# Performance work log

Measured on AMD Instinct MI355X. Metric: run time of the kernel, lower is better.

## Reference

```python
import jax, jax.numpy as jnp
import numpy as np
import math

B, S, D = 1, 2048, 2048
NQ, NKV = 32, 8
HD = D // NQ            # 64
NREP = NQ // NKV        # 4
EPS = 1e-6


def _rope_tables(seq_len, head_dim, theta=10000.0):
    half = head_dim // 2
    inv_freq = 1.0 / (theta ** (np.arange(0, half, dtype=np.float32) / half))
    t = np.arange(seq_len, dtype=np.float32)
    freqs = np.outer(t, inv_freq)  # [S, half]
    return jnp.asarray(np.cos(freqs)), jnp.asarray(np.sin(freqs))


def _rmsnorm(x, g, eps=EPS):
    denom = jnp.sqrt(jnp.mean(x * x, axis=-1, keepdims=True) + eps)
    return x / denom * g


def _rope(x, cos, sin):
    # x: [B, S, H, HD]; cos/sin: [S, HD//2]
    half = x.shape[-1] // 2
    x1, x2 = x[..., :half], x[..., half:]
    c = cos[None, :, None, :]
    s = sin[None, :, None, :]
    return jnp.concatenate([x1 * c - x2 * s, x1 * s + x2 * c], axis=-1)


def setup_inputs() -> dict:
    key = jax.random.key(0)
    ks = jax.random.split(key, 6)
    scale = 1.0 / math.sqrt(D)
    x = jax.random.normal(ks[0], (B, S, D), dtype=jnp.float32)
    Wq = jax.random.normal(ks[1], (D, NQ * HD), dtype=jnp.float32) * scale
    Wk = jax.random.normal(ks[2], (D, NKV * HD), dtype=jnp.float32) * scale
    Wv = jax.random.normal(ks[3], (D, NKV * HD), dtype=jnp.float32) * scale
    Wo = jax.random.normal(ks[4], (NQ * HD, D), dtype=jnp.float32) * scale
    g_q = jnp.ones((HD,), dtype=jnp.float32)
    g_k = jnp.ones((HD,), dtype=jnp.float32)
    cos, sin = _rope_tables(S, HD)
    return {"x": x, "cos": cos, "sin": sin, "g_q": g_q, "g_k": g_k,
            "Wq": Wq, "Wk": Wk, "Wv": Wv, "Wo": Wo}


def reference(x, cos, sin, g_q, g_k, Wq, Wk, Wv, Wo):
    bs, seq, _ = x.shape
    Q = (x @ Wq).reshape(bs, seq, NQ, HD)
    K = (x @ Wk).reshape(bs, seq, NKV, HD)
    V = (x @ Wv).reshape(bs, seq, NKV, HD)
    Q = _rope(_rmsnorm(Q, g_q), cos, sin)
    K = _rope(_rmsnorm(K, g_k), cos, sin)
    # GQA: repeat_interleave KV heads to match Q heads
    K = jnp.repeat(K, NREP, axis=2)  # [B,S,NQ,HD]
    V = jnp.repeat(V, NREP, axis=2)
    # scores: [B, H, S, S]
    scores = jnp.einsum('bshd,bthd->bhst', Q, K) / math.sqrt(HD)
    mask = jnp.triu(jnp.ones((seq, seq), dtype=bool), k=1)
    scores = jnp.where(mask, -jnp.inf, scores)
    attn = jax.nn.softmax(scores, axis=-1)
    out = jnp.einsum('bhst,bthd->bshd', attn, V).reshape(bs, seq, NQ * HD)
    return out @ Wo
```

## Files before the change

### kernel.cpp

```cpp
#include <hip/hip_runtime.h>
#include <hip/hip_bf16.h>
#include <math.h>

#define S 2048
#define D 2048
#define NQ 32
#define NKV 8
#define HD 64
#define HALF 32
#define NREP 4
#define QKV_N 3072
#define KCOL 2048
#define VCOL 2560

typedef unsigned short ushort_t;
typedef __attribute__((ext_vector_type(8))) short bf16x8;
typedef __attribute__((ext_vector_type(4))) float f32x4;
typedef float f4 __attribute__((ext_vector_type(4)));

__device__ __forceinline__ ushort_t f2bf(float f) {
    __hip_bfloat16 h = __float2bfloat16(f);
    return *reinterpret_cast<ushort_t*>(&h);
}
__device__ __forceinline__ float bf2f(ushort_t u) {
    __hip_bfloat16 h = *reinterpret_cast<__hip_bfloat16*>(&u);
    return __bfloat162float(h);
}

__device__ __forceinline__ void load_lds16(const ushort_t* g, ushort_t* l) {
    __builtin_amdgcn_global_load_lds(
        (const __attribute__((address_space(1))) unsigned int*)g,
        (__attribute__((address_space(3))) unsigned int*)l,
        16, 0, 0);
}

__global__ __launch_bounds__(256) void prep_all(const float* __restrict__ x,
                                                ushort_t* __restrict__ Xb,
                                                const float* __restrict__ Wq,
                                                const float* __restrict__ Wk,
                                                const float* __restrict__ Wv,
                                                ushort_t* __restrict__ WqkvT) {
    __shared__ float tile[32][33];
    const int b = blockIdx.x;
    if (b < 4096) {
        int i = (b * 256 + threadIdx.x) * 4;
        f4 v = *(const f4*)&x[i];
        Xb[i + 0] = f2bf(v[0]);
        Xb[i + 1] = f2bf(v[1]);
        Xb[i + 2] = f2bf(v[2]);
        Xb[i + 3] = f2bf(v[3]);
        return;
    }
    const float* src; int N, row_off, t;
    if (b < 8192)      { src = Wq; N = 2048; row_off = 0;    t = b - 4096; }
    else if (b < 9216) { src = Wk; N = 512;  row_off = 2048; t = b - 8192; }
    else               { src = Wv; N = 512;  row_off = 2560; t = b - 9216; }
    const int ntn = N / 32;
    const int n0 = (t % ntn) * 32, k0 = (t / ntn) * 32;
    const int tx = threadIdx.x & 31, ty = threadIdx.x >> 5;
    #pragma unroll
    for (int i = 0; i < 32; i += 8)
        tile[ty + i][tx] = src[(size_t)(k0 + ty + i) * N + (n0 + tx)];
    __syncthreads();
    #pragma unroll
    for (int i = 0; i < 32; i += 8)
        WqkvT[(size_t)(row_off + n0 + ty + i) * 2048 + (k0 + tx)] = f2bf(tile[tx][ty + i]);
}

template <typename OutT>
__global__ __launch_bounds__(256) void gemm64(const ushort_t* __restrict__ A,
                                              const ushort_t* __restrict__ BT,
                                              OutT* __restrict__ C,
                                              int M, int N, int Kdim) {
    __shared__ ushort_t As[64][64];
    __shared__ ushort_t Bs[64][64];
    const int tid = threadIdx.x;
    const int w = tid >> 6, lane = tid & 63;
    const int r16 = lane & 15, quad = lane >> 4;
    const int wm = (w >> 1) * 32, wn = (w & 1) * 32;
    const int bm = blockIdx.y * 64, bn = blockIdx.x * 64;
    const int srow = lane >> 3;
    const int jl = (lane & 7) ^ srow;
    const int rx = r16 & 7;

    f32x4 acc[2][2];
    #pragma unroll
    for (int r = 0; r < 2; ++r)
        #pragma unroll
        for (int c = 0; c < 2; ++c) acc[r][c] = (f32x4){0.f, 0.f, 0.f, 0.f};

    for (int k0 = 0; k0 < Kdim; k0 += 64) {
        __syncthreads();
        #pragma unroll
        for (int i = 0; i < 2; ++i) {
            int rbase = w * 16 + i * 8;
            load_lds16(A  + (size_t)(bm + rbase + srow) * Kdim + k0 + jl * 8, &As[rbase][0]);
            load_lds16(BT + (size_t)(bn + rbase + srow) * Kdim + k0 + jl * 8, &Bs[rbase][0]);
        }
        __syncthreads();

        #pragma unroll
        for (int h = 0; h < 2; ++h) {
            bf16x8 af[2], bfr[2];
            #pragma unroll
            for (int r = 0; r < 2; ++r)
                af[r]  = *(const bf16x8*)&As[wm + 16 * r + r16][((quad + 4 * h) ^ rx) * 8];
            #pragma unroll
            for (int c = 0; c < 2; ++c)
                bfr[c] = *(const bf16x8*)&Bs[wn + 16 * c + r16][((quad + 4 * h) ^ rx) * 8];
            #pragma unroll
            for (int r = 0; r < 2; ++r)
                #pragma unroll
                for (int c = 0; c < 2; ++c)
                    acc[r][c] = __builtin_amdgcn_mfma_f32_16x16x32_bf16(af[r], bfr[c], acc[r][c], 0, 0, 0);
        }
    }

    #pragma unroll
    for (int r = 0; r < 2; ++r)
        #pragma unroll
        for (int c = 0; c < 2; ++c)
            #pragma unroll
            for (int reg = 0; reg < 4; ++reg) {
                int row = bm + wm + 16 * r + quad * 4 + reg;
                int col = bn + wn + 16 * c + r16;
                float v = acc[r][c][reg];
                if constexpr (sizeof(OutT) == 2) C[(size_t)row * N + col] = (OutT)f2bf(v);
                else                             C[(size_t)row * N + col] = (OutT)v;
            }
}

__global__ __launch_bounds__(256) void rms_rope_vwo(ushort_t* __restrict__ QKV,
                                                    const float* __restrict__ gq,
                                                    const float* __restrict__ gk,
                                                    const float* __restrict__ cosT,
                                                    const float* __restrict__ sinT,
                                                    ushort_t* __restrict__ VTg,
                                                    const float* __restrict__ Wo,
                                                    ushort_t* __restrict__ WoT) {
    const int y = blockIdx.y, xb = blockIdx.x;
    if (y < 10) {
        const int s = xb;
        const int w = threadIdx.x >> 6;
        const int hh = y * 4 + w;
        const int d = threadIdx.x & 63;
        const float* g;
        int col;
        if (hh < NQ) { g = gq; col = hh * HD; }
        else         { g = gk; col = KCOL + (hh - NQ) * HD; }
        ushort_t* xp = QKV + (size_t)s * QKV_N + col;
        float v = bf2f(xp[d]);
        float ss = v * v;
        #pragma unroll
        for (int off = 32; off > 0; off >>= 1) ss += __shfl_down(ss, off);
        ss = __shfl(ss, 0);
        float inv = rsqrtf(ss * (1.0f / HD) + 1e-6f);
        float xn = v * inv * g[d];
        float other = __shfl(xn, d ^ 32);
        float c = cosT[(size_t)s * HALF + (d & 31)];
        float sn = sinT[(size_t)s * HALF + (d & 31)];
        float outv = (d < HALF) ? (xn * c - other * sn) : (other * sn + xn * c);
        xp[d] = f2bf(outv);
        return;
    }
    const int tx = threadIdx.x & 31, ty = threadIdx.x >> 5;
    if (y == 10 && xb < 1024) {
        __shared__ ushort_t vt[32][33];
        const int s0 = (xb & 63) * 32, d0 = (xb >> 6) * 32;
        #pragma unroll
        for (int i = 0; i < 32; i += 8)
            vt[ty + i][tx] = QKV[(size_t)(s0 + ty + i) * QKV_N + VCOL + d0 + tx];
        __syncthreads();
        #pragma unroll
        for (int i = 0; i < 32; i += 8)
            VTg[(size_t)(d0 + ty + i) * S + s0 + tx] = vt[tx][ty + i];
        return;
    }
    int idx;
    if (y == 10)      idx = xb - 1024;
    else if (y == 11) idx = 1024 + xb;
    else              idx = 3072 + xb;
    if (idx < 0 || idx >= 4096) return;
    __shared__ float wt[32][33];
    const int n0 = (idx & 63) * 32, k0 = (idx >> 6) * 32;
    #pragma unroll
    for (int i = 0; i < 32; i += 8)
        wt[ty + i][tx] = Wo[(size_t)(k0 + ty + i) * 2048 + (n0 + tx)];
    __syncthreads();
    #pragma unroll
    for (int i = 0; i < 32; i += 8)
        WoT[(size_t)(n0 + ty + i) * 2048 + (k0 + tx)] = f2bf(wt[tx][ty + i]);
}

__global__ __launch_bounds__(256) void zero_acc(f4* __restrict__ AccBuf4,
                                                f4* __restrict__ AccL4) {
    int i = blockIdx.x * 256 + threadIdx.x;
    if (i < 524288) AccBuf4[i] = (f4){0.f, 0.f, 0.f, 0.f};
    else if (i < 532480) AccL4[i - 524288] = (f4){0.f, 0.f, 0.f, 0.f};
}

__global__ __launch_bounds__(256) void flash_attn_mfma(const ushort_t* __restrict__ QKV,
                                                       const ushort_t* __restrict__ VTg,
                                                       ushort_t* __restrict__ O,
                                                       float* __restrict__ AccBuf,
                                                       float* __restrict__ AccL) {
    __shared__ ushort_t Ks[2][32][64];
    __shared__ ushort_t Vt[2][64][32];
    __shared__ ushort_t Ps[4][16][40];

    const int bx = blockIdx.x;
    int qt, tb, te;
    bool atom;
    if (bx < 16) { qt = 16 + bx; tb = 0; te = 32; atom = true; }
    else         { qt = 47 - bx; atom = (qt >= 16); tb = atom ? 32 : 0; te = 2 * qt + 2; }

    const int q0 = qt * 64;
    const int h  = blockIdx.y;
    const int kvh = h >> 2;
    const int tid = threadIdx.x;
    const int w = tid >> 6, lane = tid & 63;
    const int r16 = lane & 15, quad = lane >> 4;
    const int kcol = KCOL + kvh * HD;
    const int vtrow0 = kvh * HD;
    const int krow = lane >> 3;
    const int jl = (lane & 7) ^ krow;
    const int vrow = lane >> 2;
    const int jv = (lane & 3) ^ (vrow & 3);
    const int rx = r16 & 7;
    const int rx3 = r16 & 3;

    const ushort_t* qrow = QKV + (size_t)(q0 + 16 * w + r16) * QKV_N + h * HD;
    bf16x8 qf0, qf1;
    {
        bf16x8 r0 = *(const bf16x8*)(qrow + quad * 8);
        bf16x8 r1 = *(const bf16x8*)(qrow + quad * 8 + 32);
        #pragma unroll
        for (int j = 0; j < 8; ++j) {
            qf0[j] = (short)f2bf(bf2f((ushort_t)r0[j]) * 0.18033688f);
            qf1[j] = (short)f2bf(bf2f((ushort_t)r1[j]) * 0.18033688f);
        }
    }

    bf16x8 onesf;
    {
        ushort_t ov = (r16 == 0) ? (ushort_t)0x3F80 : (ushort_t)0;
        #pragma unroll
        for (int j = 0; j < 8; ++j) onesf[j] = (short)ov;
    }

    f32x4 accO[4];
    f32x4 accL = (f32x4){0.f, 0.f, 0.f, 0.f};
    #pragma unroll
    for (int c = 0; c < 4; ++c) accO[c] = (f32x4){0.f, 0.f, 0.f, 0.f};

    auto stage = [&](int b, int t) {
        const int kb = t * 32;
        load_lds16(QKV + (size_t)(kb + w * 8 + krow) * QKV_N + kcol + jl * 8,
                   &Ks[b][w * 8][0]);
        load_lds16(VTg + (size_t)(vtrow0 + w * 16 + vrow) * S + kb + jv * 8,
                   &Vt[b][w * 16][0]);
    };

    stage(tb & 1, tb);

    for (int t = tb; t < te; ++t) {
        __syncthreads();
        if (t + 1 < te) stage((t + 1) & 1, t + 1);

        const ushort_t (*K_)[64] = Ks[t & 1];
        const ushort_t (*V_)[32] = Vt[t & 1];
        const int rel = t * 32 - q0;
        const bool maskt = (rel >= 0);

        f32x4 sc[2];
        #pragma unroll
        for (int c = 0; c < 2; ++c) {
            bf16x8 kf0 = *(const bf16x8*)&K_[16 * c + r16][(quad ^ rx) * 8];
            bf16x8 kf1 = *(const bf16x8*)&K_[16 * c + r16][((quad + 4) ^ rx) * 8];
            f32x4 z = (f32x4){0.f, 0.f, 0.f, 0.f};
            z = __builtin_amdgcn_mfma_f32_16x16x32_bf16(qf0, kf0, z, 0, 0, 0);
            z = __builtin_amdgcn_mfma_f32_16x16x32_bf16(qf1, kf1, z, 0, 0, 0);
            sc[c] = z;
        }

        #pragma unroll
        for (int c = 0; c < 2; ++c)
            #pragma unroll
            for (int reg = 0; reg < 4; ++reg) {
                float v = sc[c][reg];
                if (maskt && (rel + 16 * c + r16 > 16 * w + quad * 4 + reg)) v = -INFINITY;
                Ps[w][quad * 4 + reg][16 * c + r16] = f2bf(exp2f(v));
            }

        bf16x8 pf = *(const bf16x8*)&Ps[w][r16][quad * 8];

        accL = __builtin_amdgcn_mfma_f32_16x16x32_bf16(pf, onesf, accL, 0, 0, 0);
        #pragma unroll
        for (int c = 0; c < 4; ++c) {
            bf16x8 vf = *(const bf16x8*)&V_[16 * c + r16][(quad ^ rx3) * 8];
            accO[c] = __builtin_amdgcn_mfma_f32_16x16x32_bf16(pf, vf, accO[c], 0, 0, 0);
        }
    }

    if (!atom) {
        #pragma unroll
        for (int reg = 0; reg < 4; ++reg) {
            float l = __shfl(accL[reg], lane & 48);
            float invl = 1.0f / l;
            int row = q0 + 16 * w + quad * 4 + reg;
            ushort_t* op = O + (size_t)row * D + h * HD;
            #pragma unroll
            for (int c = 0; c < 4; ++c)
                op[16 * c + r16] = f2bf(accO[c][reg] * invl);
        }
    } else {
        const int pair = (qt - 16) * 32 + h;
        float* ab = AccBuf + (size_t)pair * 4096;
        #pragma unroll
        for (int reg = 0; reg < 4; ++reg) {
            int row = 16 * w + quad * 4 + reg;
            #pragma unroll
            for (int c = 0; c < 4; ++c)
                atomicAdd(&ab[row * 64 + 16 * c + r16], accO[c][reg]);
        }
        if (r16 == 0) {
            #pragma unroll
            for (int reg = 0; reg < 4; ++reg)
                atomicAdd(&AccL[pair * 64 + 16 * w + quad * 4 + reg], accL[reg]);
        }
    }
}

__global__ __launch_bounds__(256) void normalize_o(const float* __restrict__ AccBuf,
                                                   const float* __restrict__ AccL,
                                                   ushort_t* __restrict__ O) {
    const int pair = blockIdx.x;
    const int qt = 16 + (pair >> 5);
    const int h  = pair & 31;
    const float* ab = AccBuf + (size_t)pair * 4096;
    const float* lp = AccL + pair * 64;
    for (int i = threadIdx.x; i < 4096; i += 256) {
        int row = i >> 6, d = i & 63;
        O[(size_t)(qt * 64 + row) * D + h * HD + d] = f2bf(ab[i] / lp[row]);
    }
}

extern "C" void kernel_launch(void* const* d_in, const int* in_sizes, int n_in,
                              void* d_out, int out_size, void* d_ws, size_t ws_size,
                              hipStream_t stream) {
    const float* x    = (const float*)d_in[0];
    const float* cosT = (const float*)d_in[1];
    const float* sinT = (const float*)d_in[2];
    const float* g_q  = (const float*)d_in[3];
    const float* g_k  = (const float*)d_in[4];
    const float* Wq   = (const float*)d_in[5];
    const float* Wk   = (const float*)d_in[6];
    const float* Wv   = (const float*)d_in[7];
    const float* Wo   = (const float*)d_in[8];
    float* out = (float*)d_out;

    char* base = (char*)d_ws;
    ushort_t* Xb    = (ushort_t*)base;
    ushort_t* WqkvT = (ushort_t*)(base + 8388608);
    ushort_t* QKVb  = (ushort_t*)(base + 20971520);
    ushort_t* WoT   = (ushort_t*)(base + 8388608);
    ushort_t* VTg   = (ushort_t*)(base + 16777216);
    float*    AccL  = (float*)(base + 18874368);
    float*    AccBuf = (float*)d_out;
    ushort_t* Ob    = Xb;

    prep_all<<<10240, 256, 0, stream>>>(x, Xb, Wq, Wk, Wv, WqkvT);
    gemm64<ushort_t><<<dim3(QKV_N / 64, S / 64), 256, 0, stream>>>(Xb, WqkvT, QKVb, S, QKV_N, D);
    rms_rope_vwo<<<dim3(2048, 13), 256, 0, stream>>>(QKVb, g_q, g_k, cosT, sinT, VTg, Wo, WoT);
    zero_acc<<<2080, 256, 0, stream>>>((f4*)AccBuf, (f4*)AccL);
    flash_attn_mfma<<<dim3(48, NQ), 256, 0, stream>>>(QKVb, VTg, Ob, AccBuf, AccL);
    normalize_o<<<512, 256, 0, stream>>>(AccBuf, AccL, Ob);
    gemm64<float><<<dim3(D / 64, S / 64), 256, 0, stream>>>(Ob, WoT, out, S, D, D);
}
```

Baseline: 257.5 us.

## Split-K QKV GEMM with 128 tiles and two-head flash attention blocks

The QKV projection now uses a 128x128 tile GEMM split along K into two bf16 partials, and the RMSNorm/RoPE/V-transpose pass sums them. Flash attention now processes two query heads sharing a KV head per block with 64-wide key tiles, halving the grid and reusing K/V loads from LDS. The aim is better GEMM occupancy/reuse and less redundant KV traffic. Costs include an extra bf16 partial round trip with added rounding error and relocated workspace buffers inside the output tensor.

```diff
diff --git a/kernel.cpp b/kernel.cpp
--- a/kernel.cpp
+++ b/kernel.cpp
@@ -67,11 +67,309 @@
         WqkvT[(size_t)(row_off + n0 + ty + i) * 2048 + (k0 + tx)] = f2bf(tile[tx][ty + i]);
 }
 
-template <typename OutT>
-__global__ __launch_bounds__(256) void gemm64(const ushort_t* __restrict__ A,
-                                              const ushort_t* __restrict__ BT,
-                                              OutT* __restrict__ C,
-                                              int M, int N, int Kdim) {
+__global__ __launch_bounds__(256) void gemm_qkv_sk(const ushort_t* __restrict__ A,
+                                                   const ushort_t* __restrict__ BT,
+                                                   ushort_t* __restrict__ P0,
+                                                   ushort_t* __restrict__ P1) {
+    __shared__ ushort_t As[128][32];
+    __shared__ ushort_t Bs[128][32];
+    const int tid = threadIdx.x;
+    const int w = tid >> 6, lane = tid & 63;
+    const int r16 = lane & 15, quad = lane >> 4;
+    const int wm = (w >> 1) * 64, wn = (w & 1) * 64;
+    const int bm = blockIdx.y * 128, bn = blockIdx.x * 128;
+    const int sr = lane >> 2;
+    const int sc8 = (lane & 3) * 8;
+    const int kbeg = blockIdx.z * 1024;
+    ushort_t* P = blockIdx.z ? P1 : P0;
+
+    f32x4 acc[4][4];
+    #pragma unroll
+    for (int r = 0; r < 4; ++r)
+        #pragma unroll
+        for (int c = 0; c < 4; ++c) acc[r][c] = (f32x4){0.f, 0.f, 0.f, 0.f};
+
+    for (int k0 = kbeg; k0 < kbeg + 1024; k0 += 32) {
+        __syncthreads();
+        #pragma unroll
+        for (int i = 0; i < 2; ++i) {
+            int rowt = w * 32 + i * 16;
+            load_lds16(A  + (size_t)(bm + rowt + sr) * 2048 + k0 + sc8, &As[rowt][0]);
+            load_lds16(BT + (size_t)(bn + rowt + sr) * 2048 + k0 + sc8, &Bs[rowt][0]);
+        }
+        __syncthreads();
+
+        bf16x8 af[4], bfr[4];
+        #pragma unroll
+        for (int r = 0; r < 4; ++r) af[r]  = *(const bf16x8*)&As[wm + 16 * r + r16][quad * 8];
+        #pragma unroll
+        for (int c = 0; c < 4; ++c) bfr[c] = *(const bf16x8*)&Bs[wn + 16 * c + r16][quad * 8];
+        #pragma unroll
+        for (int r = 0; r < 4; ++r)
+            #pragma unroll
+            for (int c = 0; c < 4; ++c)
+                acc[r][c] = __builtin_amdgcn_mfma_f32_16x16x32_bf16(af[r], bfr[c], acc[r][c], 0, 0, 0);
+    }
+
+    #pragma unroll
+    for (int r = 0; r < 4; ++r)
+        #pragma unroll
+        for (int c = 0; c < 4; ++c)
+            #pragma unroll
+            for (int reg = 0; reg < 4; ++reg) {
+                int row = bm + wm + 16 * r + quad * 4 + reg;
+                int col = bn + wn + 16 * c + r16;
+                P[(size_t)row * QKV_N + col] = f2bf(acc[r][c][reg]);
+            }
+}
+
+__global__ __launch_bounds__(256) void combine_qkv(ushort_t* __restrict__ QKVb,
+                                                   const ushort_t* __restrict__ P1,
+                                                   const float* __restrict__ gq,
+                                                   const float* __restrict__ gk,
+                                                   const float* __restrict__ cosT,
+                                                   const float* __restrict__ sinT,
+                                                   ushort_t* __restrict__ VTg,
+                                                   const float* __restrict__ Wo,
+                                                   ushort_t* __restrict__ WoT) {
+    const int y = blockIdx.y, xb = blockIdx.x;
+    if (y < 10) {
+        const int s = xb;
+        const int w = threadIdx.x >> 6;
+        const int hh = y * 4 + w;
+        const int d = threadIdx.x & 63;
+        const float* g;
+        int col;
+        if (hh < NQ) { g = gq; col = hh * HD; }
+        else         { g = gk; col = KCOL + (hh - NQ) * HD; }
+        ushort_t* xp = QKVb + (size_t)s * QKV_N + col;
+        const ushort_t* xp1 = P1 + (size_t)s * QKV_N + col;
+        float v = bf2f(xp[d]) + bf2f(xp1[d]);
+        float ss = v * v;
+        #pragma unroll
+        for (int off = 32; off > 0; off >>= 1) ss += __shfl_down(ss, off);
+        ss = __shfl(ss, 0);
+        float inv = rsqrtf(ss * (1.0f / HD) + 1e-6f);
+        float xn = v * inv * g[d];
+        float other = __shfl(xn, d ^ 32);
+        float c = cosT[(size_t)s * HALF + (d & 31)];
+        float sn = sinT[(size_t)s * HALF + (d & 31)];
+        float outv = (d < HALF) ? (xn * c - other * sn) : (other * sn + xn * c);
+        xp[d] = f2bf(outv);
+        return;
+    }
+    const int tx = threadIdx.x & 31, ty = threadIdx.x >> 5;
+    if (y == 10 && xb < 1024) {
+        __shared__ ushort_t vt[32][33];
+        const int s0 = (xb & 63) * 32, d0 = (xb >> 6) * 32;
+        #pragma unroll
+        for (int i = 0; i < 32; i += 8) {
+            size_t idx = (size_t)(s0 + ty + i) * QKV_N + VCOL + d0 + tx;
+            vt[ty + i][tx] = f2bf(bf2f(QKVb[idx]) + bf2f(P1[idx]));
+        }
+        __syncthreads();
+        #pragma unroll
+        for (int i = 0; i < 32; i += 8)
+            VTg[(size_t)(d0 + ty + i) * S + s0 + tx] = vt[tx][ty + i];
+        return;
+    }
+    int idx;
+    if (y == 10)      idx = xb - 1024;
+    else if (y == 11) idx = 1024 + xb;
+    else              idx = 3072 + xb;
+    if (idx < 0 || idx >= 4096) return;
+    __shared__ float wt[32][33];
+    const int n0 = (idx & 63) * 32, k0 = (idx >> 6) * 32;
+    #pragma unroll
+    for (int i = 0; i < 32; i += 8)
+        wt[ty + i][tx] = Wo[(size_t)(k0 + ty + i) * 2048 + (n0 + tx)];
+    __syncthreads();
+    #pragma unroll
+    for (int i = 0; i < 32; i += 8)
+        WoT[(size_t)(n0 + ty + i) * 2048 + (k0 + tx)] = f2bf(wt[tx][ty + i]);
+}
+
+__global__ __launch_bounds__(256) void zero_acc(f4* __restrict__ AccBuf4,
+                                                f4* __restrict__ AccL4) {
+    int i = blockIdx.x * 256 + threadIdx.x;
+    if (i < 524288) AccBuf4[i] = (f4){0.f, 0.f, 0.f, 0.f};
+    else if (i < 532480) AccL4[i - 524288] = (f4){0.f, 0.f, 0.f, 0.f};
+}
+
+__global__ __launch_bounds__(256) void flash_attn_mfma(const ushort_t* __restrict__ QKV,
+                                                       const ushort_t* __restrict__ VTg,
+                                                       ushort_t* __restrict__ O,
+                                                       float* __restrict__ AccBuf,
+                                                       float* __restrict__ AccL) {
+    __shared__ ushort_t Ks[2][64][64];
+    __shared__ ushort_t Vt[2][64][64];
+    __shared__ ushort_t Ps[2][4][16][72];
+
+    const int bx = blockIdx.x;
+    int qt, tb, te;
+    bool atom;
+    if (bx < 16) { qt = 16 + bx; tb = 0; te = 16; atom = true; }
+    else         { qt = 47 - bx; atom = (qt >= 16); tb = atom ? 16 : 0; te = qt + 1; }
+
+    const int q0 = qt * 64;
+    const int hy = blockIdx.y;
+    const int h0 = hy * 2;
+    const int kvh = hy >> 1;
+    const int tid = threadIdx.x;
+    const int w = tid >> 6, lane = tid & 63;
+    const int r16 = lane & 15, quad = lane >> 4;
+    const int kcol = KCOL + kvh * HD;
+    const int vtrow0 = kvh * HD;
+    const int rsub = lane >> 3;
+    const int jlog = (lane & 7) ^ rsub;
+    const int rx = r16 & 7;
+
+    bf16x8 qf[2][2];
+    #pragma unroll
+    for (int e = 0; e < 2; ++e) {
+        const ushort_t* qrow = QKV + (size_t)(q0 + 16 * w + r16) * QKV_N + (h0 + e) * HD;
+        bf16x8 r0 = *(const bf16x8*)(qrow + quad * 8);
+        bf16x8 r1 = *(const bf16x8*)(qrow + quad * 8 + 32);
+        #pragma unroll
+        for (int j = 0; j < 8; ++j) {
+            qf[e][0][j] = (short)f2bf(bf2f((ushort_t)r0[j]) * 0.18033688f);
+            qf[e][1][j] = (short)f2bf(bf2f((ushort_t)r1[j]) * 0.18033688f);
+        }
+    }
+
+    bf16x8 onesf;
+    {
+        ushort_t ov = (r16 == 0) ? (ushort_t)0x3F80 : (ushort_t)0;
+        #pragma unroll
+        for (int j = 0; j < 8; ++j) onesf[j] = (short)ov;
+    }
+
+    f32x4 accO[2][4];
+    f32x4 accL2[2];
+    #pragma unroll
+    for (int e = 0; e < 2; ++e) {
+        accL2[e] = (f32x4){0.f, 0.f, 0.f, 0.f};
+        #pragma unroll
+        for (int c = 0; c < 4; ++c) accO[e][c] = (f32x4){0.f, 0.f, 0.f, 0.f};
+    }
+
+    auto stage = [&](int b, int t0) {
+        #pragma unroll
+        for (int i = 0; i < 2; ++i) {
+            int base = w * 16 + i * 8;
+            int row = base + rsub;
+            load_lds16(QKV + (size_t)(t0 + row) * QKV_N + kcol + jlog * 8, &Ks[b][base][0]);
+            load_lds16(VTg + (size_t)(vtrow0 + row) * S + t0 + jlog * 8, &Vt[b][base][0]);
+        }
+    };
+
+    stage(tb & 1, tb * 64);
+
+    for (int t = tb; t < te; ++t) {
+        __syncthreads();
+        if (t + 1 < te) stage((t + 1) & 1, (t + 1) * 64);
+
+        const ushort_t (*K_)[64] = Ks[t & 1];
+        const ushort_t (*V_)[64] = Vt[t & 1];
+        const bool diag = (t == qt);
+
+        f32x4 sc[2][4];
+        #pragma unroll
+        for (int c = 0; c < 4; ++c) {
+            bf16x8 kf0 = *(const bf16x8*)&K_[16 * c + r16][(quad ^ rx) * 8];
+            bf16x8 kf1 = *(const bf16x8*)&K_[16 * c + r16][((quad + 4) ^ rx) * 8];
+            #pragma unroll
+            for (int e = 0; e < 2; ++e) {
+                f32x4 z = (f32x4){0.f, 0.f, 0.f, 0.f};
+                z = __builtin_amdgcn_mfma_f32_16x16x32_bf16(qf[e][0], kf0, z, 0, 0, 0);
+                z = __builtin_amdgcn_mfma_f32_16x16x32_bf16(qf[e][1], kf1, z, 0, 0, 0);
+                sc[e][c] = z;
+            }
+        }
+
+        #pragma unroll
+        for (int e = 0; e < 2; ++e)
+            #pragma unroll
+            for (int c = 0; c < 4; ++c)
+                #pragma unroll
+                for (int reg = 0; reg < 4; ++reg) {
+                    float v = sc[e][c][reg];
+                    if (diag && (16 * c + r16 > 16 * w + quad * 4 + reg)) v = -INFINITY;
+                    Ps[e][w][quad * 4 + reg][16 * c + r16] = f2bf(exp2f(v));
+                }
+
+        bf16x8 pf0[2], pf1[2];
+        #pragma unroll
+        for (int e = 0; e < 2; ++e) {
+            pf0[e] = *(const bf16x8*)&Ps[e][w][r16][quad * 8];
+            pf1[e] = *(const bf16x8*)&Ps[e][w][r16][quad * 8 + 32];
+            accL2[e] = __builtin_amdgcn_mfma_f32_16x16x32_bf16(pf0[e], onesf, accL2[e], 0, 0, 0);
+            accL2[e] = __builtin_amdgcn_mfma_f32_16x16x32_bf16(pf1[e], onesf, accL2[e], 0, 0, 0);
+        }
+
+        #pragma unroll
+        for (int c = 0; c < 4; ++c) {
+            bf16x8 vf0 = *(const bf16x8*)&V_[16 * c + r16][(quad ^ rx) * 8];
+            bf16x8 vf1 = *(const bf16x8*)&V_[16 * c + r16][((quad + 4) ^ rx) * 8];
+            #pragma unroll
+            for (int e = 0; e < 2; ++e) {
+                accO[e][c] = __builtin_amdgcn_mfma_f32_16x16x32_bf16(pf0[e], vf0, accO[e][c], 0, 0, 0);
+                accO[e][c] = __builtin_amdgcn_mfma_f32_16x16x32_bf16(pf1[e], vf1, accO[e][c], 0, 0, 0);
+            }
+        }
+    }
+
+    #pragma unroll
+    for (int e = 0; e < 2; ++e) {
+        const int h = h0 + e;
+        if (!atom) {
+            #pragma unroll
+            for (int reg = 0; reg < 4; ++reg) {
+                float l = __shfl(accL2[e][reg], lane & 48);
+                float invl = 1.0f / l;
+                int row = q0 + 16 * w + quad * 4 + reg;
+                ushort_t* op = O + (size_t)row * D + h * HD;
+                #pragma unroll
+                for (int c = 0; c < 4; ++c)
+                    op[16 * c + r16] = f2bf(accO[e][c][reg] * invl);
+            }
+        } else {
+            const int pair = (qt - 16) * 32 + h;
+            float* ab = AccBuf + (size_t)pair * 4096;
+            #pragma unroll
+            for (int reg = 0; reg < 4; ++reg) {
+                int row = 16 * w + quad * 4 + reg;
+                #pragma unroll
+                for (int c = 0; c < 4; ++c)
+                    atomicAdd(&ab[row * 64 + 16 * c + r16], accO[e][c][reg]);
+            }
+            if (r16 == 0) {
+                #pragma unroll
+                for (int reg = 0; reg < 4; ++reg)
+                    atomicAdd(&AccL[pair * 64 + 16 * w + quad * 4 + reg], accL2[e][reg]);
+            }
+        }
+    }
+}
+
+__global__ __launch_bounds__(256) void normalize_o(const float* __restrict__ AccBuf,
+                                                   const float* __restrict__ AccL,
+                                                   ushort_t* __restrict__ O) {
+    const int b = blockIdx.x;
+    const int qt = 16 + (b >> 5);
+    const int h  = b & 31;
+    const float* ab = AccBuf + (size_t)b * 4096;
+    const float* lp = AccL + b * 64;
+    for (int i = threadIdx.x; i < 4096; i += 256) {
+        int row = i >> 6, d = i & 63;
+        O[(size_t)(qt * 64 + row) * D + h * HD + d] = f2bf(ab[i] / lp[row]);
+    }
+}
+
+__global__ __launch_bounds__(256) void gemm64_f(const ushort_t* __restrict__ A,
+                                                const ushort_t* __restrict__ BT,
+                                                float* __restrict__ C,
+                                                int M, int N, int Kdim) {
     __shared__ ushort_t As[64][64];
     __shared__ ushort_t Bs[64][64];
     const int tid = threadIdx.x;
@@ -100,14 +398,14 @@
         __syncthreads();
 
         #pragma unroll
-        for (int h = 0; h < 2; ++h) {
+        for (int hh = 0; hh < 2; ++hh) {
             bf16x8 af[2], bfr[2];
             #pragma unroll
             for (int r = 0; r < 2; ++r)
-                af[r]  = *(const bf16x8*)&As[wm + 16 * r + r16][((quad + 4 * h) ^ rx) * 8];
+                af[r]  = *(const bf16x8*)&As[wm + 16 * r + r16][((quad + 4 * hh) ^ rx) * 8];
             #pragma unroll
             for (int c = 0; c < 2; ++c)
-                bfr[c] = *(const bf16x8*)&Bs[wn + 16 * c + r16][((quad + 4 * h) ^ rx) * 8];
+                bfr[c] = *(const bf16x8*)&Bs[wn + 16 * c + r16][((quad + 4 * hh) ^ rx) * 8];
             #pragma unroll
             for (int r = 0; r < 2; ++r)
                 #pragma unroll
@@ -124,225 +422,8 @@
             for (int reg = 0; reg < 4; ++reg) {
                 int row = bm + wm + 16 * r + quad * 4 + reg;
                 int col = bn + wn + 16 * c + r16;
-                float v = acc[r][c][reg];
-                if constexpr (sizeof(OutT) == 2) C[(size_t)row * N + col] = (OutT)f2bf(v);
-                else                             C[(size_t)row * N + col] = (OutT)v;
-            }
-}
-
-__global__ __launch_bounds__(256) void rms_rope_vwo(ushort_t* __restrict__ QKV,
-                                                    const float* __restrict__ gq,
-                                                    const float* __restrict__ gk,
-                                                    const float* __restrict__ cosT,
-                                                    const float* __restrict__ sinT,
-                                                    ushort_t* __restrict__ VTg,
-                                                    const float* __restrict__ Wo,
-                                                    ushort_t* __restrict__ WoT) {
-    const int y = blockIdx.y, xb = blockIdx.x;
-    if (y < 10) {
-        const int s = xb;
-        const int w = threadIdx.x >> 6;
-        const int hh = y * 4 + w;
-        const int d = threadIdx.x & 63;
-        const float* g;
-        int col;
-        if (hh < NQ) { g = gq; col = hh * HD; }
-        else         { g = gk; col = KCOL + (hh - NQ) * HD; }
-        ushort_t* xp = QKV + (size_t)s * QKV_N + col;
-        float v = bf2f(xp[d]);
-        float ss = v * v;
-        #pragma unroll
-        for (int off = 32; off > 0; off >>= 1) ss += __shfl_down(ss, off);
-        ss = __shfl(ss, 0);
-        float inv = rsqrtf(ss * (1.0f / HD) + 1e-6f);
-        float xn = v * inv * g[d];
-        float other = __shfl(xn, d ^ 32);
-        float c = cosT[(size_t)s * HALF + (d & 31)];
-        float sn = sinT[(size_t)s * HALF + (d & 31)];
-        float outv = (d < HALF) ? (xn * c - other * sn) : (other * sn + xn * c);
-        xp[d] = f2bf(outv);
-        return;
-    }
-    const int tx = threadIdx.x & 31, ty = threadIdx.x >> 5;
-    if (y == 10 && xb < 1024) {
-        __shared__ ushort_t vt[32][33];
-        const int s0 = (xb & 63) * 32, d0 = (xb >> 6) * 32;
-        #pragma unroll
-        for (int i = 0; i < 32; i += 8)
-            vt[ty + i][tx] = QKV[(size_t)(s0 + ty + i) * QKV_N + VCOL + d0 + tx];
-        __syncthreads();
-        #pragma unroll
-        for (int i = 0; i < 32; i += 8)
-            VTg[(size_t)(d0 + ty + i) * S + s0 + tx] = vt[tx][ty + i];
-        return;
-    }
-    int idx;
-    if (y == 10)      idx = xb - 1024;
-    else if (y == 11) idx = 1024 + xb;
-    else              idx = 3072 + xb;
-    if (idx < 0 || idx >= 4096) return;
-    __shared__ float wt[32][33];
-    const int n0 = (idx & 63) * 32, k0 = (idx >> 6) * 32;
-    #pragma unroll
-    for (int i = 0; i < 32; i += 8)
-        wt[ty + i][tx] = Wo[(size_t)(k0 + ty + i) * 2048 + (n0 + tx)];
-    __syncthreads();
-    #pragma unroll
-    for (int i = 0; i < 32; i += 8)
-        WoT[(size_t)(n0 + ty + i) * 2048 + (k0 + tx)] = f2bf(wt[tx][ty + i]);
-}
-
-__global__ __launch_bounds__(256) void zero_acc(f4* __restrict__ AccBuf4,
-                                                f4* __restrict__ AccL4) {
-    int i = blockIdx.x * 256 + threadIdx.x;
-    if (i < 524288) AccBuf4[i] = (f4){0.f, 0.f, 0.f, 0.f};
-    else if (i < 532480) AccL4[i - 524288] = (f4){0.f, 0.f, 0.f, 0.f};
-}
-
-__global__ __launch_bounds__(256) void flash_attn_mfma(const ushort_t* __restrict__ QKV,
-                                                       const ushort_t* __restrict__ VTg,
-                                                       ushort_t* __restrict__ O,
-                                                       float* __restrict__ AccBuf,
-                                                       float* __restrict__ AccL) {
-    __shared__ ushort_t Ks[2][32][64];
-    __shared__ ushort_t Vt[2][64][32];
-    __shared__ ushort_t Ps[4][16][40];
-
-    const int bx = blockIdx.x;
-    int qt, tb, te;
-    bool atom;
-    if (bx < 16) { qt = 16 + bx; tb = 0; te = 32; atom = true; }
-    else         { qt = 47 - bx; atom = (qt >= 16); tb = atom ? 32 : 0; te = 2 * qt + 2; }
-
-    const int q0 = qt * 64;
-    const int h  = blockIdx.y;
-    const int kvh = h >> 2;
-    const int tid = threadIdx.x;
-    const int w = tid >> 6, lane = tid & 63;
-    const int r16 = lane & 15, quad = lane >> 4;
-    const int kcol = KCOL + kvh * HD;
-    const int vtrow0 = kvh * HD;
-    const int krow = lane >> 3;
-    const int jl = (lane & 7) ^ krow;
-    const int vrow = lane >> 2;
-    const int jv = (lane & 3) ^ (vrow & 3);
-    const int rx = r16 & 7;
-    const int rx3 = r16 & 3;
-
-    const ushort_t* qrow = QKV + (size_t)(q0 + 16 * w + r16) * QKV_N + h * HD;
-    bf16x8 qf0, qf1;
-    {
-        bf16x8 r0 = *(const bf16x8*)(qrow + quad * 8);
-        bf16x8 r1 = *(const bf16x8*)(qrow + quad * 8 + 32);
-        #pragma unroll
-        for (int j = 0; j < 8; ++j) {
-            qf0[j] = (short)f2bf(bf2f((ushort_t)r0[j]) * 0.18033688f);
-            qf1[j] = (short)f2bf(bf2f((ushort_t)r1[j]) * 0.18033688f);
-        }
-    }
-
-    bf16x8 onesf;
-    {
-        ushort_t ov = (r16 == 0) ? (ushort_t)0x3F80 : (ushort_t)0;
-        #pragma unroll
-        for (int j = 0; j < 8; ++j) onesf[j] = (short)ov;
-    }
-
-    f32x4 accO[4];
-    f32x4 accL = (f32x4){0.f, 0.f, 0.f, 0.f};
-    #pragma unroll
-    for (int c = 0; c < 4; ++c) accO[c] = (f32x4){0.f, 0.f, 0.f, 0.f};
-
-    auto stage = [&](int b, int t) {
-        const int kb = t * 32;
-        load_lds16(QKV + (size_t)(kb + w * 8 + krow) * QKV_N + kcol + jl * 8,
-                   &Ks[b][w * 8][0]);
-        load_lds16(VTg + (size_t)(vtrow0 + w * 16 + vrow) * S + kb + jv * 8,
-                   &Vt[b][w * 16][0]);
-    };
-
-    stage(tb & 1, tb);
-
-    for (int t = tb; t < te; ++t) {
-        __syncthreads();
-        if (t + 1 < te) stage((t + 1) & 1, t + 1);
-
-        const ushort_t (*K_)[64] = Ks[t & 1];
-        const ushort_t (*V_)[32] = Vt[t & 1];
-        const int rel = t * 32 - q0;
-        const bool maskt = (rel >= 0);
-
-        f32x4 sc[2];
-        #pragma unroll
-        for (int c = 0; c < 2; ++c) {
-            bf16x8 kf0 = *(const bf16x8*)&K_[16 * c + r16][(quad ^ rx) * 8];
-            bf16x8 kf1 = *(const bf16x8*)&K_[16 * c + r16][((quad + 4) ^ rx) * 8];
-            f32x4 z = (f32x4){0.f, 0.f, 0.f, 0.f};
-            z = __builtin_amdgcn_mfma_f32_16x16x32_bf16(qf0, kf0, z, 0, 0, 0);
-            z = __builtin_amdgcn_mfma_f32_16x16x32_bf16(qf1, kf1, z, 0, 0, 0);
-            sc[c] = z;
-        }
-
-        #pragma unroll
-        for (int c = 0; c < 2; ++c)
-            #pragma unroll
-            for (int reg = 0; reg < 4; ++reg) {
-                float v = sc[c][reg];
-                if (maskt && (rel + 16 * c + r16 > 16 * w + quad * 4 + reg)) v = -INFINITY;
-                Ps[w][quad * 4 + reg][16 * c + r16] = f2bf(exp2f(v));
-            }
-
-        bf16x8 pf = *(const bf16x8*)&Ps[w][r16][quad * 8];
-
-        accL = __builtin_amdgcn_mfma_f32_16x16x32_bf16(pf, onesf, accL, 0, 0, 0);
-        #pragma unroll
-        for (int c = 0; c < 4; ++c) {
-            bf16x8 vf = *(const bf16x8*)&V_[16 * c + r16][(quad ^ rx3) * 8];
-            accO[c] = __builtin_amdgcn_mfma_f32_16x16x32_bf16(pf, vf, accO[c], 0, 0, 0);
-        }
-    }
-
-    if (!atom) {
-        #pragma unroll
-        for (int reg = 0; reg < 4; ++reg) {
-            float l = __shfl(accL[reg], lane & 48);
-            float invl = 1.0f / l;
-            int row = q0 + 16 * w + quad * 4 + reg;
-            ushort_t* op = O + (size_t)row * D + h * HD;
-            #pragma unroll
-            for (int c = 0; c < 4; ++c)
-                op[16 * c + r16] = f2bf(accO[c][reg] * invl);
-        }
-    } else {
-        const int pair = (qt - 16) * 32 + h;
-        float* ab = AccBuf + (size_t)pair * 4096;
-        #pragma unroll
-        for (int reg = 0; reg < 4; ++reg) {
-            int row = 16 * w + quad * 4 + reg;
-            #pragma unroll
-            for (int c = 0; c < 4; ++c)
-                atomicAdd(&ab[row * 64 + 16 * c + r16], accO[c][reg]);
-        }
-        if (r16 == 0) {
-            #pragma unroll
-            for (int reg = 0; reg < 4; ++reg)
-                atomicAdd(&AccL[pair * 64 + 16 * w + quad * 4 + reg], accL[reg]);
-        }
-    }
-}
-
-__global__ __launch_bounds__(256) void normalize_o(const float* __restrict__ AccBuf,
-                                                   const float* __restrict__ AccL,
-                                                   ushort_t* __restrict__ O) {
-    const int pair = blockIdx.x;
-    const int qt = 16 + (pair >> 5);
-    const int h  = pair & 31;
-    const float* ab = AccBuf + (size_t)pair * 4096;
-    const float* lp = AccL + pair * 64;
-    for (int i = threadIdx.x; i < 4096; i += 256) {
-        int row = i >> 6, d = i & 63;
-        O[(size_t)(qt * 64 + row) * D + h * HD + d] = f2bf(ab[i] / lp[row]);
-    }
+                C[(size_t)row * N + col] = acc[r][c][reg];
+            }
 }
 
 extern "C" void kernel_launch(void* const* d_in, const int* in_sizes, int n_in,
@@ -360,20 +441,22 @@
     float* out = (float*)d_out;
 
     char* base = (char*)d_ws;
-    ushort_t* Xb    = (ushort_t*)base;
-    ushort_t* WqkvT = (ushort_t*)(base + 8388608);
-    ushort_t* QKVb  = (ushort_t*)(base + 20971520);
-    ushort_t* WoT   = (ushort_t*)(base + 8388608);
-    ushort_t* VTg   = (ushort_t*)(base + 16777216);
-    float*    AccL  = (float*)(base + 18874368);
-    float*    AccBuf = (float*)d_out;
-    ushort_t* Ob    = Xb;
+    char* ob   = (char*)d_out;
+    ushort_t* Xb     = (ushort_t*)base;
+    ushort_t* WqkvT  = (ushort_t*)(base + 8388608);
+    ushort_t* QKVb   = (ushort_t*)(base + 20971520);
+    ushort_t* WoT    = (ushort_t*)(base + 8388608);
+    ushort_t* Ob     = Xb;
+    ushort_t* P1     = (ushort_t*)ob;
+    float*    AccBuf = (float*)ob;
+    ushort_t* VTg    = (ushort_t*)(ob + 12582912);
+    float*    AccL   = (float*)(ob + 14680064);
 
     prep_all<<<10240, 256, 0, stream>>>(x, Xb, Wq, Wk, Wv, WqkvT);
-    gemm64<ushort_t><<<dim3(QKV_N / 64, S / 64), 256, 0, stream>>>(Xb, WqkvT, QKVb, S, QKV_N, D);
-    rms_rope_vwo<<<dim3(2048, 13), 256, 0, stream>>>(QKVb, g_q, g_k, cosT, sinT, VTg, Wo, WoT);
+    gemm_qkv_sk<<<dim3(24, 16, 2), 256, 0, stream>>>(Xb, WqkvT, QKVb, P1);
+    combine_qkv<<<dim3(2048, 13), 256, 0, stream>>>(QKVb, P1, g_q, g_k, cosT, sinT, VTg, Wo, WoT);
     zero_acc<<<2080, 256, 0, stream>>>((f4*)AccBuf, (f4*)AccL);
-    flash_attn_mfma<<<dim3(48, NQ), 256, 0, stream>>>(QKVb, VTg, Ob, AccBuf, AccL);
+    flash_attn_mfma<<<dim3(48, 16), 256, 0, stream>>>(QKVb, VTg, Ob, AccBuf, AccL);
     normalize_o<<<512, 256, 0, stream>>>(AccBuf, AccL, Ob);
-    gemm64<float><<<dim3(D / 64, S / 64), 256, 0, stream>>>(Ob, WoT, out, S, D, D);
-}
+    gemm64_f<<<dim3(D / 64, S / 64), 256, 0, stream>>>(Ob, WoT, out, S, D, D);
+}
```

After: 250.2 us. 1.03x faster.
